# Kernel optimization log

Hardware: AMD Instinct MI355X
Metric: run time of the kernel (lower is better)

## Reference

```python
import jax, jax.numpy as jnp
import numpy as np

D_MODEL = 768
N_HEADS = 12
D_K = D_MODEL // N_HEADS


def setup_inputs() -> dict:
    key = jax.random.key(0)
    k_x, k_wqkv, k_bqkv, k_wo, k_bo = jax.random.split(key, 5)
    s = 1.0 / np.sqrt(D_MODEL)
    return {
        "x": jax.random.normal(k_x, (2, 4096, D_MODEL), dtype=jnp.float32),
        "w_qkv": jax.random.uniform(k_wqkv, (D_MODEL, 3 * D_MODEL), jnp.float32, -s, s),
        "b_qkv": jax.random.uniform(k_bqkv, (3 * D_MODEL,), jnp.float32, -s, s),
        "w_out": jax.random.uniform(k_wo, (D_MODEL, D_MODEL), jnp.float32, -s, s),
        "b_out": jax.random.uniform(k_bo, (D_MODEL,), jnp.float32, -s, s),
    }


def reference(x, w_qkv, b_qkv, w_out, b_out):
    B, S, E = x.shape
    qkv = x @ w_qkv + b_qkv                                  # [B,S,3E]
    qkv = qkv.reshape(B, S, 3, N_HEADS, D_K)
    qkv = jnp.transpose(qkv, (2, 0, 3, 1, 4))                # [3,B,H,S,Dk]
    q, k, v = qkv[0], qkv[1], qkv[2]
    scores = jnp.einsum("bhsd,bhtd->bhst", q, k) / jnp.sqrt(jnp.float32(D_K))
    attn = jax.nn.softmax(scores, axis=-1)                   # [B,H,S,S]
    ctx = jnp.einsum("bhst,bhtd->bhsd", attn, v)             # [B,H,S,Dk]
    ctx = jnp.transpose(ctx, (0, 2, 1, 3)).reshape(B, S, E)  # [B,S,E]
    return ctx @ w_out + b_out
```

## Files before the change

### kernel.cpp

```cpp
#include <hip/hip_runtime.h>

typedef short short8 __attribute__((ext_vector_type(8)));
typedef float f32x4 __attribute__((ext_vector_type(4)));
typedef float f32x16 __attribute__((ext_vector_type(16)));
typedef unsigned short u16;
typedef unsigned int u32;

__device__ __forceinline__ u16 f2bf(float f) {
  u32 u = __float_as_uint(f);
  u32 r = u + 0x7fffu + ((u >> 16) & 1u);
  return (u16)(r >> 16);
}

__device__ __forceinline__ u32 cvtpk(float lo, float hi) {
  u32 r;
  asm("v_cvt_pk_bf16_f32 %0, %1, %2" : "=v"(r) : "v"(lo), "v"(hi));
  return r;
}

__device__ __forceinline__ void async_copy16(u16* lds_dst, const u16* gsrc) {
  __builtin_amdgcn_global_load_lds(
      (const __attribute__((address_space(1))) u32*)gsrc,
      (__attribute__((address_space(3))) u32*)lds_dst, 16, 0, 0);
}

__global__ void cvt_f32_bf16(const float4* __restrict__ in, uint2* __restrict__ out, int n4) {
  int i = blockIdx.x * blockDim.x + threadIdx.x;
  if (i >= n4) return;
  float4 v = in[i];
  uint2 o;
  o.x = (u32)f2bf(v.x) | ((u32)f2bf(v.y) << 16);
  o.y = (u32)f2bf(v.z) | ((u32)f2bf(v.w) << 16);
  out[i] = o;
}

__global__ __launch_bounds__(256) void cvt_transpose_w(
    const float* __restrict__ W, u16* __restrict__ WT, int K, int N) {
  __shared__ float tl[32 * 33];
  int n0 = blockIdx.x * 32, k0 = blockIdx.y * 32;
  int tx = threadIdx.x & 31, ty = threadIdx.x >> 5;
#pragma unroll
  for (int j = 0; j < 4; ++j)
    tl[(ty + j * 8) * 33 + tx] = W[(size_t)(k0 + ty + j * 8) * N + n0 + tx];
  __syncthreads();
#pragma unroll
  for (int j = 0; j < 4; ++j)
    WT[(size_t)(n0 + ty + j * 8) * K + k0 + tx] = f2bf(tl[tx * 33 + ty + j * 8]);
}

__global__ __launch_bounds__(256) void transpose_v(
    const u16* __restrict__ V, u16* __restrict__ VT) {
  __shared__ u16 tb[64 * 66];
  const int tid = threadIdx.x;
  const int bh = blockIdx.y;
  const int t0 = blockIdx.x * 64;
  const u16* Vb = V + (size_t)bh * 4096 * 64;
  u16* VTb = VT + (size_t)bh * 64 * 4096;
#pragma unroll
  for (int it = 0; it < 2; ++it) {
    int cid = it * 256 + tid;
    int row = cid >> 3, c = cid & 7;
    short8 v = *(const short8*)&Vb[(size_t)(t0 + row) * 64 + c * 8];
#pragma unroll
    for (int i = 0; i < 8; ++i) tb[row * 66 + c * 8 + i] = (u16)v[i];
  }
  __syncthreads();
#pragma unroll
  for (int it = 0; it < 2; ++it) {
    int pid = it * 256 + tid;
    int c2 = pid & 7, d = pid >> 3;
    short8 o;
#pragma unroll
    for (int i = 0; i < 8; ++i) o[i] = (short)tb[(c2 * 8 + i) * 66 + d];
    *(short8*)&VTb[(size_t)d * 4096 + t0 + c2 * 8] = o;
  }
}

#define BM 128
#define BN 128
#define BKG 64

template <int EPI>
__global__ __launch_bounds__(256, 2) void gemm_bf16(
    const u16* __restrict__ A, const u16* __restrict__ Bt,
    const float* __restrict__ bias, int M, int N, int K,
    u16* __restrict__ q_out, u16* __restrict__ k_out, u16* __restrict__ v_out,
    float* __restrict__ c_out) {
  __shared__ u16 lA[BM * BKG];
  __shared__ u16 lB[BN * BKG];
  const int tid = threadIdx.x;
  const int lane = tid & 63;
  const int wid = tid >> 6;
  const int r = lane & 15, hi = lane >> 4;
  const int m0 = blockIdx.y * BM;
  const int n0 = blockIdx.x * BN;
  const int wm = (wid >> 1) * 64;
  const int wn = (wid & 1) * 64;

  f32x4 acc[4][4];
#pragma unroll
  for (int i = 0; i < 4; ++i)
#pragma unroll
    for (int j = 0; j < 4; ++j) acc[i][j] = f32x4{0.f, 0.f, 0.f, 0.f};

  for (int k0 = 0; k0 < K; k0 += BKG) {
#pragma unroll
    for (int j = 0; j < 4; ++j) {
      int cid = j * 256 + tid;
      int row = cid >> 3, c = cid & 7;
      async_copy16(&lA[cid * 8], &A[(size_t)(m0 + row) * K + k0 + c * 8]);
    }
#pragma unroll
    for (int j = 0; j < 4; ++j) {
      int cid = j * 256 + tid;
      int row = cid >> 3, c = cid & 7;
      async_copy16(&lB[cid * 8], &Bt[(size_t)(n0 + row) * K + k0 + c * 8]);
    }
    __syncthreads();
#pragma unroll
    for (int kk = 0; kk < 2; ++kk) {
      short8 af[4], bfr[4];
#pragma unroll
      for (int i = 0; i < 4; ++i)
        af[i] = *(const short8*)&lA[(wm + i * 16 + r) * BKG + kk * 32 + hi * 8];
#pragma unroll
      for (int i = 0; i < 4; ++i)
        bfr[i] = *(const short8*)&lB[(wn + i * 16 + r) * BKG + kk * 32 + hi * 8];
#pragma unroll
      for (int i = 0; i < 4; ++i)
#pragma unroll
        for (int j = 0; j < 4; ++j)
          acc[i][j] = __builtin_amdgcn_mfma_f32_16x16x32_bf16(af[i], bfr[j], acc[i][j], 0, 0, 0);
    }
    __syncthreads();
  }

#pragma unroll
  for (int i = 0; i < 4; ++i) {
#pragma unroll
    for (int j = 0; j < 4; ++j) {
      int gn = n0 + wn + j * 16 + r;
      float bv = bias[gn];
#pragma unroll
      for (int q = 0; q < 4; ++q) {
        int gm = m0 + wm + i * 16 + hi * 4 + q;
        float v = acc[i][j][q] + bv;
        if (EPI == 0) {
          int part = gn / 768;
          int rem = gn - part * 768;
          int h = rem >> 6, d = rem & 63;
          int b = gm >> 12, s = gm & 4095;
          size_t off = (((size_t)(b * 12 + h) * 4096) + s) * 64 + d;
          if (part == 0) q_out[off] = f2bf(v * 0.18033688011112042f);
          else if (part == 1) k_out[off] = f2bf(v);
          else v_out[off] = f2bf(v);
        } else {
          c_out[(size_t)gm * N + gn] = v;
        }
      }
    }
  }
}

__global__ __launch_bounds__(256, 3) void attn_fwd(
    const u16* __restrict__ Qg, const u16* __restrict__ Kg,
    const u16* __restrict__ VTg, u16* __restrict__ ctxg) {
  __shared__ u16 lK[2][64 * 64];
  __shared__ u16 lV[2][64 * 64];
  const int tid = threadIdx.x;
  const int lane = tid & 63, wid = tid >> 6;
  const int q32 = lane & 31, half = lane >> 5;
  const int bh = blockIdx.y;
  const int s0 = blockIdx.x * 128;
  const int qrow = s0 + wid * 32 + q32;
  const u16* Qb = Qg + (size_t)bh * 4096 * 64;
  const u16* Kb = Kg + (size_t)bh * 4096 * 64;
  const u16* Vb = VTg + (size_t)bh * 64 * 4096;
  const int xorq = q32 & 7;

  short8 qf[4];
#pragma unroll
  for (int dc = 0; dc < 4; ++dc)
    qf[dc] = *(const short8*)&Qb[(size_t)qrow * 64 + dc * 16 + half * 8];

  int offlo[4], offhi[4];
#pragma unroll
  for (int i = 0; i < 4; ++i) {
    offlo[i] = q32 * 128 + (((i * 2 + half) ^ xorq) << 4);
    offhi[i] = offlo[i] + 32 * 128;
  }

  const int srow = tid >> 3, schk = (tid & 7) ^ ((tid >> 3) & 7);
  const u16* kp0 = Kb + srow * 64 + schk * 8;
  const u16* kp1 = kp0 + 32 * 64;
  const u16* vp0 = Vb + (size_t)srow * 4096 + schk * 8;
  const u16* vp1 = vp0 + (size_t)32 * 4096;

  f32x16 zc;
#pragma unroll
  for (int i = 0; i < 16; ++i) zc[i] = 0.f;

  f32x16 acc0, acc1;
#pragma unroll
  for (int i = 0; i < 16; ++i) { acc0[i] = 0.f; acc1[i] = 0.f; }
  float l_run = 0.f;

#define STAGE(buf, t0_)                                            \
  do {                                                             \
    async_copy16(&lK[buf][tid * 8], kp0 + (t0_) * 64);             \
    async_copy16(&lK[buf][(256 + tid) * 8], kp1 + (t0_) * 64);     \
    async_copy16(&lV[buf][tid * 8], vp0 + (t0_));                  \
    async_copy16(&lV[buf][(256 + tid) * 8], vp1 + (t0_));          \
  } while (0)

#define PV_KS(KS)                                                              \
  {                                                                            \
    u32 x0 = w0[2 * (KS)], y0 = w0[2 * (KS) + 1];                              \
    u32 x1 = w1[2 * (KS)], y1 = w1[2 * (KS) + 1];                              \
    asm("v_permlane32_swap_b32 %0, %1" : "+v"(x0), "+v"(y0));                  \
    asm("v_permlane32_swap_b32 %0, %1" : "+v"(x1), "+v"(y1));                  \
    union { u32 u[4]; short8 s; } pa;                                          \
    pa.u[0] = x0; pa.u[1] = x1; pa.u[2] = y0; pa.u[3] = y1;                    \
    {                                                                          \
      short8 vf = *(const short8*)(lVc + offlo[KS]);                           \
      acc0 = __builtin_amdgcn_mfma_f32_32x32x16_bf16(pa.s, vf, acc0, 0, 0, 0); \
    }                                                                          \
    {                                                                          \
      short8 vf = *(const short8*)(lVc + offhi[KS]);                           \
      acc1 = __builtin_amdgcn_mfma_f32_32x32x16_bf16(pa.s, vf, acc1, 0, 0, 0); \
    }                                                                          \
  }

#define SM_HALF(S, WOFF)                                                       \
  _Pragma("unroll") for (int g = 0; g < 4; ++g) {                              \
    float e0 = exp2f(S[4 * g + 0]), e1 = exp2f(S[4 * g + 1]);                  \
    float e2 = exp2f(S[4 * g + 2]), e3 = exp2f(S[4 * g + 3]);                  \
    w0[(WOFF) + g] = cvtpk(e0, e1);                                            \
    w1[(WOFF) + g] = cvtpk(e2, e3);                                            \
    ps0 += e0; ps1 += e1; ps2 += e2; ps3 += e3;                                \
  }

#define ATTN_TILE(CUR, T0)                                                     \
  {                                                                            \
    __syncthreads();                                                           \
    if ((T0) + 64 < 4096) STAGE((CUR) ^ 1, (T0) + 64);                         \
    const char* lKc = (const char*)lK[CUR];                                    \
    const char* lVc = (const char*)lV[CUR];                                    \
    f32x16 sA, sB;                                                             \
    {                                                                          \
      short8 kA = *(const short8*)(lKc + offlo[0]);                            \
      sA = __builtin_amdgcn_mfma_f32_32x32x16_bf16(kA, qf[0], zc, 0, 0, 0);    \
    }                                                                          \
    _Pragma("unroll") for (int dc = 1; dc < 4; ++dc) {                         \
      short8 kA = *(const short8*)(lKc + offlo[dc]);                           \
      sA = __builtin_amdgcn_mfma_f32_32x32x16_bf16(kA, qf[dc], sA, 0, 0, 0);   \
    }                                                                          \
    {                                                                          \
      short8 kB = *(const short8*)(lKc + offhi[0]);                            \
      sB = __builtin_amdgcn_mfma_f32_32x32x16_bf16(kB, qf[0], zc, 0, 0, 0);    \
    }                                                                          \
    _Pragma("unroll") for (int dc = 1; dc < 4; ++dc) {                         \
      short8 kB = *(const short8*)(lKc + offhi[dc]);                           \
      sB = __builtin_amdgcn_mfma_f32_32x32x16_bf16(kB, qf[dc], sB, 0, 0, 0);   \
    }                                                                          \
    u32 w0[8], w1[8];                                                          \
    float ps0 = 0.f, ps1 = 0.f, ps2 = 0.f, ps3 = 0.f;                          \
    SM_HALF(sA, 0)                                 \
    PV_KS(0)                                                                   \
    PV_KS(1)                                                                   \
    SM_HALF(sB, 4)                              \
    PV_KS(2)                                                                   \
    PV_KS(3)                                                                   \
    l_run += (ps0 + ps1) + (ps2 + ps3);                                        \
  }

  STAGE(0, 0);
  for (int t0 = 0; t0 < 4096; t0 += 128) {
    ATTN_TILE(0, t0);
    ATTN_TILE(1, t0 + 64);
  }

  float l_tot = l_run + __shfl_xor(l_run, 32);
  float inv = 1.f / l_tot;
  int b = bh / 12, h = bh - b * 12;
#pragma unroll
  for (int reg = 0; reg < 16; ++reg) {
    int row = (reg & 3) + 8 * (reg >> 2) + 4 * half;
    float iv = __shfl(inv, row);
    size_t base = ((size_t)b * 4096 + s0 + wid * 32 + row) * 768 + h * 64;
    ctxg[base + q32] = f2bf(acc0[reg] * iv);
    ctxg[base + 32 + q32] = f2bf(acc1[reg] * iv);
  }
}

extern "C" void kernel_launch(void* const* d_in, const int* in_sizes, int n_in,
                              void* d_out, int out_size, void* d_ws, size_t ws_size,
                              hipStream_t stream) {
  const float* x = (const float*)d_in[0];
  const float* w_qkv = (const float*)d_in[1];
  const float* b_qkv = (const float*)d_in[2];
  const float* w_out = (const float*)d_in[3];
  const float* b_out = (const float*)d_in[4];
  float* out = (float*)d_out;

  char* ws = (char*)d_ws;
  const size_t SZ_X = (size_t)8192 * 768 * 2;
  const size_t SZ_WQ = (size_t)2304 * 768 * 2;
  const size_t SZ_WO = (size_t)768 * 768 * 2;
  const size_t SZ_HSD = (size_t)24 * 4096 * 64 * 2;
  u16* xb = (u16*)ws;     ws += SZ_X;
  u16* wqkvT = (u16*)ws;  ws += SZ_WQ;
  u16* woutT = (u16*)ws;  ws += SZ_WO;
  u16* Qb = (u16*)ws;     ws += SZ_HSD;
  u16* Kb = (u16*)ws;     ws += SZ_HSD;
  u16* Vb = (u16*)ws;     ws += SZ_HSD;
  u16* VTb = (u16*)ws;    ws += SZ_HSD;
  u16* ctxb = (u16*)ws;   ws += SZ_X;

  cvt_f32_bf16<<<dim3(6144), dim3(256), 0, stream>>>(
      (const float4*)x, (uint2*)xb, 8192 * 768 / 4);
  cvt_transpose_w<<<dim3(72, 24), dim3(256), 0, stream>>>(w_qkv, wqkvT, 768, 2304);
  cvt_transpose_w<<<dim3(24, 24), dim3(256), 0, stream>>>(w_out, woutT, 768, 768);
  gemm_bf16<0><<<dim3(18, 64), dim3(256), 0, stream>>>(
      xb, wqkvT, b_qkv, 8192, 2304, 768, Qb, Kb, Vb, (float*)nullptr);
  transpose_v<<<dim3(64, 24), dim3(256), 0, stream>>>(Vb, VTb);
  attn_fwd<<<dim3(32, 24), dim3(256), 0, stream>>>(Qb, Kb, VTb, ctxb);
  gemm_bf16<1><<<dim3(6, 64), dim3(256), 0, stream>>>(
      ctxb, woutT, b_out, 8192, 768, 768, (u16*)nullptr, (u16*)nullptr, (u16*)nullptr, out);
}
```

Before: 244.8 us.

## Fuse V transpose into QKV GEMM epilogue and compute softmax sum via MFMA

The QKV GEMM epilogue now writes V directly in transposed [B,H,D,S] layout, removing the separate transpose kernel and its intermediate buffer. In attention, the softmax denominator is accumulated by an extra MFMA of the probability tile against a ones vector instead of scalar adds plus cross-lane shuffles. This trades VALU work for additional matrix-core work and makes the V stores in the GEMM epilogue strided, which may hurt coalescing.

```diff
diff --git a/kernel.cpp b/kernel.cpp
--- a/kernel.cpp
+++ b/kernel.cpp
@@ -48,34 +48,6 @@
     WT[(size_t)(n0 + ty + j * 8) * K + k0 + tx] = f2bf(tl[tx * 33 + ty + j * 8]);
 }
 
-__global__ __launch_bounds__(256) void transpose_v(
-    const u16* __restrict__ V, u16* __restrict__ VT) {
-  __shared__ u16 tb[64 * 66];
-  const int tid = threadIdx.x;
-  const int bh = blockIdx.y;
-  const int t0 = blockIdx.x * 64;
-  const u16* Vb = V + (size_t)bh * 4096 * 64;
-  u16* VTb = VT + (size_t)bh * 64 * 4096;
-#pragma unroll
-  for (int it = 0; it < 2; ++it) {
-    int cid = it * 256 + tid;
-    int row = cid >> 3, c = cid & 7;
-    short8 v = *(const short8*)&Vb[(size_t)(t0 + row) * 64 + c * 8];
-#pragma unroll
-    for (int i = 0; i < 8; ++i) tb[row * 66 + c * 8 + i] = (u16)v[i];
-  }
-  __syncthreads();
-#pragma unroll
-  for (int it = 0; it < 2; ++it) {
-    int pid = it * 256 + tid;
-    int c2 = pid & 7, d = pid >> 3;
-    short8 o;
-#pragma unroll
-    for (int i = 0; i < 8; ++i) o[i] = (short)tb[(c2 * 8 + i) * 66 + d];
-    *(short8*)&VTb[(size_t)d * 4096 + t0 + c2 * 8] = o;
-  }
-}
-
 #define BM 128
 #define BN 128
 #define BKG 64
@@ -84,7 +56,7 @@
 __global__ __launch_bounds__(256, 2) void gemm_bf16(
     const u16* __restrict__ A, const u16* __restrict__ Bt,
     const float* __restrict__ bias, int M, int N, int K,
-    u16* __restrict__ q_out, u16* __restrict__ k_out, u16* __restrict__ v_out,
+    u16* __restrict__ q_out, u16* __restrict__ k_out, u16* __restrict__ vt_out,
     float* __restrict__ c_out) {
   __shared__ u16 lA[BM * BKG];
   __shared__ u16 lB[BN * BKG];
@@ -150,10 +122,16 @@
           int rem = gn - part * 768;
           int h = rem >> 6, d = rem & 63;
           int b = gm >> 12, s = gm & 4095;
-          size_t off = (((size_t)(b * 12 + h) * 4096) + s) * 64 + d;
-          if (part == 0) q_out[off] = f2bf(v * 0.18033688011112042f);
-          else if (part == 1) k_out[off] = f2bf(v);
-          else v_out[off] = f2bf(v);
+          if (part == 0) {
+            size_t off = (((size_t)(b * 12 + h) * 4096) + s) * 64 + d;
+            q_out[off] = f2bf(v * 0.18033688011112042f);
+          } else if (part == 1) {
+            size_t off = (((size_t)(b * 12 + h) * 4096) + s) * 64 + d;
+            k_out[off] = f2bf(v);
+          } else {
+            size_t off = (((size_t)(b * 12 + h) * 64) + d) * 4096 + s;
+            vt_out[off] = f2bf(v);
+          }
         } else {
           c_out[(size_t)gm * N + gn] = v;
         }
@@ -196,14 +174,15 @@
   const u16* vp0 = Vb + (size_t)srow * 4096 + schk * 8;
   const u16* vp1 = vp0 + (size_t)32 * 4096;
 
+  const short8 ones8 = {0x3F80, 0x3F80, 0x3F80, 0x3F80,
+                        0x3F80, 0x3F80, 0x3F80, 0x3F80};
   f32x16 zc;
 #pragma unroll
   for (int i = 0; i < 16; ++i) zc[i] = 0.f;
 
-  f32x16 acc0, acc1;
-#pragma unroll
-  for (int i = 0; i < 16; ++i) { acc0[i] = 0.f; acc1[i] = 0.f; }
-  float l_run = 0.f;
+  f32x16 acc0, acc1, acc_l;
+#pragma unroll
+  for (int i = 0; i < 16; ++i) { acc0[i] = 0.f; acc1[i] = 0.f; acc_l[i] = 0.f; }
 
 #define STAGE(buf, t0_)                                            \
   do {                                                             \
@@ -229,6 +208,7 @@
       short8 vf = *(const short8*)(lVc + offhi[KS]);                           \
       acc1 = __builtin_amdgcn_mfma_f32_32x32x16_bf16(pa.s, vf, acc1, 0, 0, 0); \
     }                                                                          \
+    acc_l = __builtin_amdgcn_mfma_f32_32x32x16_bf16(pa.s, ones8, acc_l, 0, 0, 0); \
   }
 
 #define SM_HALF(S, WOFF)                                                       \
@@ -237,7 +217,6 @@
     float e2 = exp2f(S[4 * g + 2]), e3 = exp2f(S[4 * g + 3]);                  \
     w0[(WOFF) + g] = cvtpk(e0, e1);                                            \
     w1[(WOFF) + g] = cvtpk(e2, e3);                                            \
-    ps0 += e0; ps1 += e1; ps2 += e2; ps3 += e3;                                \
   }
 
 #define ATTN_TILE(CUR, T0)                                                     \
@@ -264,14 +243,12 @@
       sB = __builtin_amdgcn_mfma_f32_32x32x16_bf16(kB, qf[dc], sB, 0, 0, 0);   \
     }                                                                          \
     u32 w0[8], w1[8];                                                          \
-    float ps0 = 0.f, ps1 = 0.f, ps2 = 0.f, ps3 = 0.f;                          \
     SM_HALF(sA, 0)                                 \
     PV_KS(0)                                                                   \
     PV_KS(1)                                                                   \
     SM_HALF(sB, 4)                              \
     PV_KS(2)                                                                   \
     PV_KS(3)                                                                   \
-    l_run += (ps0 + ps1) + (ps2 + ps3);                                        \
   }
 
   STAGE(0, 0);
@@ -280,13 +257,11 @@
     ATTN_TILE(1, t0 + 64);
   }
 
-  float l_tot = l_run + __shfl_xor(l_run, 32);
-  float inv = 1.f / l_tot;
   int b = bh / 12, h = bh - b * 12;
 #pragma unroll
   for (int reg = 0; reg < 16; ++reg) {
     int row = (reg & 3) + 8 * (reg >> 2) + 4 * half;
-    float iv = __shfl(inv, row);
+    float iv = 1.f / acc_l[reg];
     size_t base = ((size_t)b * 4096 + s0 + wid * 32 + row) * 768 + h * 64;
     ctxg[base + q32] = f2bf(acc0[reg] * iv);
     ctxg[base + 32 + q32] = f2bf(acc1[reg] * iv);
@@ -313,7 +288,6 @@
   u16* woutT = (u16*)ws;  ws += SZ_WO;
   u16* Qb = (u16*)ws;     ws += SZ_HSD;
   u16* Kb = (u16*)ws;     ws += SZ_HSD;
-  u16* Vb = (u16*)ws;     ws += SZ_HSD;
   u16* VTb = (u16*)ws;    ws += SZ_HSD;
   u16* ctxb = (u16*)ws;   ws += SZ_X;
 
@@ -322,8 +296,7 @@
   cvt_transpose_w<<<dim3(72, 24), dim3(256), 0, stream>>>(w_qkv, wqkvT, 768, 2304);
   cvt_transpose_w<<<dim3(24, 24), dim3(256), 0, stream>>>(w_out, woutT, 768, 768);
   gemm_bf16<0><<<dim3(18, 64), dim3(256), 0, stream>>>(
-      xb, wqkvT, b_qkv, 8192, 2304, 768, Qb, Kb, Vb, (float*)nullptr);
-  transpose_v<<<dim3(64, 24), dim3(256), 0, stream>>>(Vb, VTb);
+      xb, wqkvT, b_qkv, 8192, 2304, 768, Qb, Kb, VTb, (float*)nullptr);
   attn_fwd<<<dim3(32, 24), dim3(256), 0, stream>>>(Qb, Kb, VTb, ctxb);
   gemm_bf16<1><<<dim3(6, 64), dim3(256), 0, stream>>>(
       ctxb, woutT, b_out, 8192, 768, 768, (u16*)nullptr, (u16*)nullptr, (u16*)nullptr, out);
```

Result: slower. 253.3 us (+3.5%).
